# Optimization experiments

Hardware: AMD Instinct MI355X
Metric: run time of the kernel (lower is better)

Reference implementation:

```python
import jax, jax.numpy as jnp
import numpy as np

B, Ng, A, Eg = 32, 2500, 50, 2000      # graphs, atoms/graph, residues/graph, edges/graph
DIN, EDIM, H1, H2, AF, HG = 64, 16, 64, 64, 95, 128
F1, F2, F3 = 64, 32, 16
K, T = 3, 6                             # ARMA num_stacks, num_layers
N, E = B * Ng, B * Eg


def _glorot(k, shape, fan_in):
    return jax.random.normal(k, shape, jnp.float32) / np.sqrt(fan_in)


def setup_inputs():
    key = jax.random.key(0)
    ks = jax.random.split(key, 24)
    x = jax.random.normal(ks[0], (N, DIN), jnp.float32)
    off = (jnp.arange(B) * Ng)[:, None]
    src = (jax.random.randint(ks[1], (B, Eg), 0, Ng) + off).reshape(-1)
    dst = (jax.random.randint(ks[2], (B, Eg), 0, Ng) + off).reshape(-1)
    edge_index = jnp.stack([src, dst])
    edge_attr = jax.random.normal(ks[3], (E, EDIM), jnp.float32)
    monomer_labels = jnp.tile(jnp.arange(Ng) // (Ng // A), B)  # atom -> residue (0..A-1, per graph)
    aminoacids_features = jax.random.normal(ks[4], (B, A, AF), jnp.float32)
    FIN = H2 + AF  # 159, ARMA input dim
    return {
        'x': x, 'edge_index': edge_index, 'edge_attr': edge_attr,
        'monomer_labels': monomer_labels, 'aminoacids_features': aminoacids_features,
        'w_e1': _glorot(ks[5], (EDIM, DIN * H1), EDIM), 'b_e1': jnp.zeros((DIN * H1,)),
        'root1': _glorot(ks[6], (DIN, H1), DIN), 'bias1': jnp.zeros((H1,)),
        'w_e2': _glorot(ks[7], (EDIM, H1 * H2), EDIM), 'b_e2': jnp.zeros((H1 * H2,)),
        'root2': _glorot(ks[8], (H1, H2), H1), 'bias2': jnp.zeros((H2,)),
        'attn_atom_w': _glorot(ks[9], (H2, 1), H2), 'attn_atom_b': jnp.zeros((1,)),
        'arma_init_w': _glorot(ks[10], (K, FIN, HG), FIN),
        'arma_w': _glorot(ks[11], (T - 1, K, HG, HG), HG),
        'arma_root_w': _glorot(ks[12], (T, K, FIN, HG), FIN),
        'arma_bias': jnp.zeros((T, K, 1, HG)),
        'attn_aa_w': _glorot(ks[13], (HG, 1), HG), 'attn_aa_b': jnp.zeros((1,)),
        'w1': _glorot(ks[14], (HG, F1), HG), 'b1': jnp.zeros((F1,)),
        'w2': _glorot(ks[15], (F1, F2), F1), 'b2': jnp.zeros((F2,)),
        'w3': _glorot(ks[16], (F2, F3), F2), 'b3': jnp.zeros((F3,)),
        'w4': _glorot(ks[17], (F3, 1), F3), 'b4': jnp.zeros((1,)),
    }


def reference(x, edge_index, edge_attr, monomer_labels, aminoacids_features,
              w_e1, b_e1, root1, bias1, w_e2, b_e2, root2, bias2,
              attn_atom_w, attn_atom_b, arma_init_w, arma_w, arma_root_w, arma_bias,
              attn_aa_w, attn_aa_b, w1, b1, w2, b2, w3, b3, w4, b4):
    src, dst = edge_index[0], edge_index[1]

    def nnconv(h, w_e, b_e, root, bias):
        din, dout = root.shape
        W = (edge_attr @ w_e + b_e).reshape(-1, din, dout)      # per-edge weight [E, din, dout]
        msg = jnp.einsum('ei,eio->eo', h[src], W)               # per-edge matvec
        agg = jax.ops.segment_sum(msg, dst, num_segments=N)     # scatter-add at dst
        return agg + h @ root + bias

    h = jax.nn.relu(nnconv(x, w_e1, b_e1, root1, bias1))
    h = jax.nn.relu(nnconv(h, w_e2, b_e2, root2, bias2))

    # AttentionReadoutAtom per graph: softmax over atoms, scatter-sum to residues
    hb = h.reshape(B, Ng, H2)
    attn = jax.nn.softmax(hb @ attn_atom_w + attn_atom_b, axis=1)
    wx = (hb * attn).reshape(-1, H2)
    seg = (monomer_labels.reshape(B, Ng) + jnp.arange(B)[:, None] * A).reshape(-1)
    amino = jax.ops.segment_sum(wx, seg, num_segments=B * A).reshape(B, A, H2)
    xi = jnp.concatenate([amino, aminoacids_features], axis=-1)  # [B, A, H2+95]

    # ARMAConv over directed residue chain i->i+1; gcn_norm w/o self-loops:
    # node 0 has in-degree 0 so edge (0,1) gets norm 0, all others norm 1.
    norm = jnp.concatenate([jnp.zeros(1), jnp.ones(A - 2)])      # [A-1]

    def prop(z):  # z: [B, K, A, F]; out[i+1] = norm_i * z[i]
        shifted = z[..., :-1, :] * norm[:, None]
        return jnp.concatenate([jnp.zeros_like(z[..., :1, :]), shifted], axis=-2)

    out = prop(jnp.einsum('baf,kfg->bkag', xi, arma_init_w))
    out = jax.nn.relu(out + jnp.einsum('baf,kfg->bkag', xi, arma_root_w[0]) + arma_bias[0][None])
    for t in range(1, T):
        out = prop(jnp.einsum('bkaf,kfg->bkag', out, arma_w[t - 1]))
        out = jax.nn.relu(out + jnp.einsum('baf,kfg->bkag', xi, arma_root_w[t]) + arma_bias[t][None])
    g = jax.nn.relu(out.mean(axis=1))  # mean over K stacks -> [B, A, HG]

    # AttentionReadoutAminoAcid: softmax over residues, weighted sum
    a = jax.nn.softmax(g @ attn_aa_w + attn_aa_b, axis=1)
    p = (g * a).sum(axis=1)  # [B, HG]

    # MLP head (dropout is identity in eval mode)
    p = jax.nn.relu(p @ w1 + b1)
    p = jax.nn.relu(p @ w2 + b2)
    p = jax.nn.relu(p @ w3 + b3)
    return (p @ w4 + b4).reshape(-1)
```

## Files before the change

### kernel.cpp

```cpp
#include <hip/hip_runtime.h>

#define N_NODES 80000
#define N_EDGES 64000
#define NB      32
#define NG      2500
#define NA      50
#define EDIM    16
#define FIN     159
#define HG      128
#define RICOLS  2688

typedef __attribute__((ext_vector_type(8))) short bf16x8;
typedef __attribute__((ext_vector_type(4))) float f32x4;

__device__ inline ushort rne_bf16(float f) {
    union { float f; unsigned u; } v; v.f = f;
    const unsigned r = v.u + 0x7fffu + ((v.u >> 16) & 1u);
    return (ushort)(r >> 16);
}
__device__ inline float bf16_to_f32(ushort h) {
    union { unsigned u; float f; } v; v.u = ((unsigned)h) << 16;
    return v.f;
}
__device__ __forceinline__ void gl_lds16(const void* gsrc, void* ldst) {
    __builtin_amdgcn_global_load_lds(
        (const __attribute__((address_space(1))) unsigned int*)gsrc,
        (__attribute__((address_space(3))) unsigned int*)ldst, 16, 0, 0);
}

__global__ __launch_bounds__(256) void prep_all(const float* __restrict__ we1, const float* __restrict__ be1,
    const float* __restrict__ we2, const float* __restrict__ be2, const float* __restrict__ armaw,
    ushort* __restrict__ w1h, ushort* __restrict__ w1l, ushort* __restrict__ w2h, ushort* __restrict__ w2l,
    ushort* __restrict__ abh, ushort* __restrict__ abl)
{
    const int b = blockIdx.x;
    if (b < 68) {
        int idx = b * 256 + threadIdx.x;
        const int half = (idx >= 17 * 8 * 64) ? 1 : 0;
        if (half) idx -= 17 * 8 * 64;
        if (idx >= 17 * 8 * 64) return;
        const float* we = half ? we2 : we1;
        const float* be = half ? be2 : be1;
        ushort* Wh = half ? w2h : w1h;
        ushort* Wlo = half ? w2l : w1l;
        const int l = idx & 63;
        const int slot = (idx >> 6) & 7;
        const int j = idx >> 9;
        const int n = slot >> 1, kq = slot & 1;
        const int o = n * 16 + (l & 15);
        const int i0 = kq * 32 + (l >> 4) * 8;
        ushort th[8], tl[8];
#pragma unroll
        for (int t = 0; t < 8; ++t) {
            const int i = i0 + t;
            const float f = (j < 16) ? we[j * 4096 + i * 64 + o] : be[i * 64 + o];
            const ushort hi = rne_bf16(f);
            th[t] = hi;
            tl[t] = rne_bf16(f - bf16_to_f32(hi));
        }
        *(uint4*)(Wh + (size_t)idx * 8) = *(const uint4*)th;
        *(uint4*)(Wlo + (size_t)idx * 8) = *(const uint4*)tl;
    } else {
        const int idx = (b - 68) * 256 + threadIdx.x;
        if (idx >= 15 * 32 * 64) return;
        const int l = idx & 63;
        const int slot = (idx >> 6) & 31;
        const int ws = idx >> 11;
        const int n = slot >> 2, kt = slot & 3;
        const int c = n * 16 + (l & 15);
        const int f0 = kt * 32 + (l >> 4) * 8;
        ushort th[8], tl[8];
#pragma unroll
        for (int t = 0; t < 8; ++t) {
            const float v = armaw[(size_t)ws * 16384 + (size_t)(f0 + t) * 128 + c];
            const ushort hi = rne_bf16(v);
            th[t] = hi;
            tl[t] = rne_bf16(v - bf16_to_f32(hi));
        }
        *(uint4*)(abh + (size_t)idx * 8) = *(const uint4*)th;
        *(uint4*)(abl + (size_t)idx * 8) = *(const uint4*)tl;
    }
}

template<int RELU>
__global__ __launch_bounds__(256) void root_gemm(const float* __restrict__ in,
    const float* __restrict__ w, const float* __restrict__ bias, float* __restrict__ out)
{
    __shared__ float At[64 * 65];
    __shared__ float Wl[64 * 64];
    __shared__ float bl[64];
    const int tid = threadIdx.x;
    const int r0 = blockIdx.x * 64;
    for (int s = tid; s < 4096; s += 256) {
        int r = s >> 6, c = s & 63;
        float v = in[(r0 + r) * 64 + c];
        if (RELU) v = fmaxf(v, 0.f);
        At[c * 65 + r] = v;
    }
    for (int s = tid; s < 4096; s += 256) Wl[s] = w[s];
    if (tid < 64) bl[tid] = bias[tid];
    __syncthreads();
    const int tr = tid >> 4, tc = tid & 15;
    float acc[4][4] = {};
#pragma unroll 8
    for (int i = 0; i < 64; ++i) {
        const float4 a4 = *(const float4*)&At[i * 65 + tr * 4];
        const float4 b4 = *(const float4*)&Wl[i * 64 + tc * 4];
        const float av[4] = {a4.x, a4.y, a4.z, a4.w};
        const float bv[4] = {b4.x, b4.y, b4.z, b4.w};
#pragma unroll
        for (int m = 0; m < 4; ++m)
#pragma unroll
            for (int n = 0; n < 4; ++n) acc[m][n] = fmaf(av[m], bv[n], acc[m][n]);
    }
    const float4 bq = *(const float4*)&bl[tc * 4];
#pragma unroll
    for (int m = 0; m < 4; ++m) {
        float4 o4 = {acc[m][0] + bq.x, acc[m][1] + bq.y, acc[m][2] + bq.z, acc[m][3] + bq.w};
        *(float4*)&out[(r0 + tr * 4 + m) * 64 + tc * 4] = o4;
    }
}

#define TE 128
template<int RELU>
__global__ __launch_bounds__(256) void edge_conv_mfma(const float* __restrict__ h,
    const float* __restrict__ ea, const int* __restrict__ src, const int* __restrict__ dst,
    const ushort* __restrict__ Whi, const ushort* __restrict__ Wlo, float* __restrict__ agg)
{
    __shared__ ushort Bst[2][8192];
    __shared__ float  EAt[17 * 132];
    const int tid = threadIdx.x;
    const int e0 = blockIdx.x * TE;
    const int wv = tid >> 6, l = tid & 63;

#pragma unroll
    for (int i = 0; i < 4; ++i) {
        const int c = wv * 4 + i;
        const ushort* gs = (c < 8) ? (Whi + ((size_t)c * 64 + l) * 8)
                                   : (Wlo + ((size_t)(c - 8) * 64 + l) * 8);
        gl_lds16(gs, (char*)(&Bst[0][0]) + c * 1024);
    }
    for (int s = tid; s < TE * 16; s += 256) {
        const int le = s >> 4, j = s & 15;
        EAt[j * 132 + le] = ea[(size_t)(e0 + le) * 16 + j];
    }
    if (tid < TE) EAt[16 * 132 + tid] = 1.0f;

    bf16x8 ah[2][2], al[2][2];
#pragma unroll
    for (int m = 0; m < 2; ++m) {
        const int erow = wv * 32 + m * 16 + (l & 15);
        const int nd = src[e0 + erow];
        const float4* hp = (const float4*)(h + (size_t)nd * 64);
#pragma unroll
        for (int kq = 0; kq < 2; ++kq) {
            const int q0 = kq * 8 + (l >> 4) * 2;
            const float4 v0 = hp[q0], v1 = hp[q0 + 1];
            const float fv[8] = {v0.x, v0.y, v0.z, v0.w, v1.x, v1.y, v1.z, v1.w};
            ushort th[8], tl[8];
#pragma unroll
            for (int t = 0; t < 8; ++t) {
                const float f = RELU ? fmaxf(fv[t], 0.f) : fv[t];
                th[t] = rne_bf16(f);
                tl[t] = rne_bf16(f - bf16_to_f32(th[t]));
            }
            ah[m][kq] = *(const bf16x8*)th;
            al[m][kq] = *(const bf16x8*)tl;
        }
    }
    __syncthreads();

    f32x4 msg[2][4];
#pragma unroll
    for (int m = 0; m < 2; ++m)
#pragma unroll
        for (int n = 0; n < 4; ++n) msg[m][n] = (f32x4)0.f;

#pragma unroll 1
    for (int j = 0; j < 17; ++j) {
        const int cur = j & 1;
        if (j < 16) {
#pragma unroll
            for (int i = 0; i < 4; ++i) {
                const int c = wv * 4 + i;
                const ushort* gs = (c < 8) ? (Whi + ((size_t)((j + 1) * 8 + c) * 64 + l) * 8)
                                           : (Wlo + ((size_t)((j + 1) * 8 + (c - 8)) * 64 + l) * 8);
                gl_lds16(gs, (char*)(&Bst[cur ^ 1][0]) + c * 1024);
            }
        }
        f32x4 eam[2];
        eam[0] = *(const f32x4*)&EAt[j * 132 + wv * 32 + (l >> 4) * 4];
        eam[1] = *(const f32x4*)&EAt[j * 132 + wv * 32 + 16 + (l >> 4) * 4];
#pragma unroll
        for (int n = 0; n < 4; ++n) {
            const char* bb = (const char*)(&Bst[cur][0]);
            const bf16x8 bh0 = *(const bf16x8*)(bb + ((n * 2 + 0) * 64 + l) * 16);
            const bf16x8 bh1 = *(const bf16x8*)(bb + ((n * 2 + 1) * 64 + l) * 16);
            const bf16x8 bl0 = *(const bf16x8*)(bb + 8192 + ((n * 2 + 0) * 64 + l) * 16);
            const bf16x8 bl1 = *(const bf16x8*)(bb + 8192 + ((n * 2 + 1) * 64 + l) * 16);
#pragma unroll
            for (int m = 0; m < 2; ++m) {
                f32x4 t = __builtin_amdgcn_mfma_f32_16x16x32_bf16(ah[m][0], bh0, (f32x4)0.f, 0, 0, 0);
                t = __builtin_amdgcn_mfma_f32_16x16x32_bf16(ah[m][1], bh1, t, 0, 0, 0);
                t = __builtin_amdgcn_mfma_f32_16x16x32_bf16(ah[m][0], bl0, t, 0, 0, 0);
                t = __builtin_amdgcn_mfma_f32_16x16x32_bf16(ah[m][1], bl1, t, 0, 0, 0);
                t = __builtin_amdgcn_mfma_f32_16x16x32_bf16(al[m][0], bh0, t, 0, 0, 0);
                t = __builtin_amdgcn_mfma_f32_16x16x32_bf16(al[m][1], bh1, t, 0, 0, 0);
                msg[m][n] += eam[m] * t;
            }
        }
        __syncthreads();
    }

#pragma unroll
    for (int m = 0; m < 2; ++m)
#pragma unroll
        for (int r = 0; r < 4; ++r) {
            const int erow = wv * 32 + m * 16 + (l >> 4) * 4 + r;
            const size_t d = (size_t)dst[e0 + erow] * 64;
#pragma unroll
            for (int n = 0; n < 4; ++n)
                atomicAdd(&agg[d + n * 16 + (l & 15)], msg[m][n][r]);
        }
}

__global__ __launch_bounds__(256) void scores_k(const float* __restrict__ h2,
    const float* __restrict__ w, const float* __restrict__ b, float* __restrict__ sc)
{
    __shared__ float wl[64];
    if (threadIdx.x < 64) wl[threadIdx.x] = w[threadIdx.x];
    __syncthreads();
    const int n = blockIdx.x * 256 + threadIdx.x;
    if (n < N_NODES) {
        float acc = b[0];
        const float4* hp = (const float4*)(h2 + (long)n * 64);
#pragma unroll
        for (int q = 0; q < 16; ++q) {
            const float4 v = hp[q];
            acc = fmaf(fmaxf(v.x, 0.f), wl[q * 4 + 0], acc); acc = fmaf(fmaxf(v.y, 0.f), wl[q * 4 + 1], acc);
            acc = fmaf(fmaxf(v.z, 0.f), wl[q * 4 + 2], acc); acc = fmaf(fmaxf(v.w, 0.f), wl[q * 4 + 3], acc);
        }
        sc[n] = acc;
    }
}

__global__ __launch_bounds__(256) void softmax_k(const float* __restrict__ sc, float* __restrict__ attn)
{
    __shared__ float red[256];
    const int g = blockIdx.x, tid = threadIdx.x;
    const float* s = sc + (long)g * NG;
    float m = -1e30f;
    for (int a = tid; a < NG; a += 256) m = fmaxf(m, s[a]);
    red[tid] = m; __syncthreads();
    for (int st = 128; st; st >>= 1) { if (tid < st) red[tid] = fmaxf(red[tid], red[tid + st]); __syncthreads(); }
    const float mx = red[0]; __syncthreads();
    float sum = 0.f;
    for (int a = tid; a < NG; a += 256) sum += expf(s[a] - mx);
    red[tid] = sum; __syncthreads();
    for (int st = 128; st; st >>= 1) { if (tid < st) red[tid] += red[tid + st]; __syncthreads(); }
    const float inv = 1.0f / red[0];
    for (int a = tid; a < NG; a += 256) attn[(long)g * NG + a] = expf(s[a] - mx) * inv;
}

__global__ __launch_bounds__(256) void amino_k(const float* __restrict__ h2,
    const float* __restrict__ attn, const float* __restrict__ aa, float* __restrict__ xi)
{
    const int tid = threadIdx.x;
    const int r = blockIdx.x * 4 + (tid >> 6);
    const int o = tid & 63;
    const int g = r / NA, ar = r % NA;
    const long base = (long)g * NG + ar * 50;
    float acc = 0.f;
#pragma unroll 10
    for (int a = 0; a < 50; ++a) acc = fmaf(attn[base + a], fmaxf(h2[(base + a) * 64 + o], 0.f), acc);
    xi[(long)r * FIN + o] = acc;
    for (int s = tid; s < 4 * 95; s += 256) {
        const int lr = s / 95, f = s % 95;
        const int rr = blockIdx.x * 4 + lr;
        xi[(long)rr * FIN + 64 + f] = aa[(long)rr * 95 + f];
    }
}

__global__ __launch_bounds__(256) void ri_gemm(const float* __restrict__ xi,
    const float* __restrict__ rootw, const float* __restrict__ initw,
    const float* __restrict__ abias, float* __restrict__ RI)
{
    __shared__ float At[32 * 65];
    __shared__ float Bl[32 * 64];
    const int tid = threadIdx.x;
    const int r0 = blockIdx.x * 64, c0 = blockIdx.y * 64;
    const int blk = c0 >> 7;
    const int gb = c0 & 127;
    const float* bsrc = (blk < 18) ? (rootw + (long)blk * FIN * 128) : (initw + (long)(blk - 18) * FIN * 128);
    const int tr = tid >> 4, tc = tid & 15;
    float acc[4][4] = {};
    for (int f0 = 0; f0 < FIN; f0 += 32) {
        __syncthreads();
        for (int s = tid; s < 64 * 32; s += 256) {
            const int r = s >> 5, kk = s & 31; const int f = f0 + kk;
            At[kk * 65 + r] = (f < FIN) ? xi[(long)(r0 + r) * FIN + f] : 0.f;
        }
        for (int s = tid; s < 32 * 64; s += 256) {
            const int kk = s >> 6, cc = s & 63; const int f = f0 + kk;
            Bl[s] = (f < FIN) ? bsrc[(long)f * 128 + gb + cc] : 0.f;
        }
        __syncthreads();
#pragma unroll 8
        for (int kk = 0; kk < 32; ++kk) {
            const float4 a4 = *(const float4*)&At[kk * 65 + tr * 4];
            const float4 b4 = *(const float4*)&Bl[kk * 64 + tc * 4];
            const float av[4] = {a4.x, a4.y, a4.z, a4.w};
            const float bv[4] = {b4.x, b4.y, b4.z, b4.w};
#pragma unroll
            for (int m = 0; m < 4; ++m)
#pragma unroll
                for (int n = 0; n < 4; ++n) acc[m][n] = fmaf(av[m], bv[n], acc[m][n]);
        }
    }
    float4 bq = {0.f, 0.f, 0.f, 0.f};
    if (blk < 18) bq = *(const float4*)&abias[c0 + tc * 4];
#pragma unroll
    for (int m = 0; m < 4; ++m) {
        float4 o4 = {acc[m][0] + bq.x, acc[m][1] + bq.y, acc[m][2] + bq.z, acc[m][3] + bq.w};
        *(float4*)&RI[(long)(r0 + tr * 4 + m) * RICOLS + c0 + tc * 4] = o4;
    }
}

__global__ __launch_bounds__(64) void arma_mfma(const float* __restrict__ RI,
    const ushort* __restrict__ Bh, const ushort* __restrict__ Bl, float* __restrict__ G)
{
    __shared__ float X[16 * 132];
    const int bid = blockIdx.x;
    const int chunk = bid % 5;
    const int gk = bid / 5;
    const int k = gk % 3, g = gk / 3;
    const int s0 = chunk * 11 - 5;
    const size_t rbase = (size_t)g * NA;
    const int l = threadIdx.x;

    for (int s = l; s < 16 * 128; s += 64) {
        const int lr = s >> 7, o = s & 127;
        const int a = s0 + lr;
        float v = 0.f;
        if (a >= 0 && a < NA) {
            v = RI[(rbase + a) * RICOLS + k * 128 + o];
            if (a >= 2) v += RI[(rbase + a - 1) * RICOLS + (18 + k) * 128 + o];
            v = fmaxf(v, 0.f);
        }
        X[lr * 132 + o] = v;
    }

    const int arow = l & 15;
    const int aabs = s0 + arow;
    const bool avalid = (arow >= 1) && (aabs >= 2) && (aabs < NA);
    const int srow = avalid ? (arow - 1) : arow;

#pragma unroll 1
    for (int t = 1; t <= 5; ++t) {
        bf16x8 ah[4], al[4];
#pragma unroll
        for (int kt = 0; kt < 4; ++kt) {
            const float* xp = &X[srow * 132 + kt * 32 + (l >> 4) * 8];
            const float4 v0 = *(const float4*)xp;
            const float4 v1 = *(const float4*)(xp + 4);
            const float fv[8] = {v0.x, v0.y, v0.z, v0.w, v1.x, v1.y, v1.z, v1.w};
            ushort th[8], tl[8];
#pragma unroll
            for (int t8 = 0; t8 < 8; ++t8) {
                const float f = avalid ? fv[t8] : 0.f;
                th[t8] = rne_bf16(f);
                tl[t8] = rne_bf16(f - bf16_to_f32(th[t8]));
            }
            ah[kt] = *(const bf16x8*)th;
            al[kt] = *(const bf16x8*)tl;
        }
        f32x4 acc[8];
#pragma unroll
        for (int n = 0; n < 8; ++n) acc[n] = (f32x4)0.f;
        const size_t wb = (size_t)(((t - 1) * 3 + k) * 32) * 512;
#pragma unroll
        for (int kt = 0; kt < 4; ++kt) {
            bf16x8 bh8[8], bl8[8];
#pragma unroll
            for (int n = 0; n < 8; ++n) {
                const size_t fo = wb + (size_t)(n * 4 + kt) * 512 + (size_t)l * 8;
                bh8[n] = *(const bf16x8*)(Bh + fo);
                bl8[n] = *(const bf16x8*)(Bl + fo);
            }
#pragma unroll
            for (int n = 0; n < 8; ++n) {
                acc[n] = __builtin_amdgcn_mfma_f32_16x16x32_bf16(ah[kt], bh8[n], acc[n], 0, 0, 0);
                acc[n] = __builtin_amdgcn_mfma_f32_16x16x32_bf16(ah[kt], bl8[n], acc[n], 0, 0, 0);
                acc[n] = __builtin_amdgcn_mfma_f32_16x16x32_bf16(al[kt], bh8[n], acc[n], 0, 0, 0);
            }
        }
#pragma unroll
        for (int n = 0; n < 8; ++n) {
            const int col = n * 16 + (l & 15);
#pragma unroll
            for (int r = 0; r < 4; ++r) {
                const int crow = (l >> 4) * 4 + r;
                const int ca = s0 + crow;
                float v = 0.f;
                if (ca >= 0 && ca < NA) {
                    const float rv = RI[(rbase + ca) * RICOLS + (t * 3 + k) * 128 + col];
                    v = fmaxf(acc[n][r] + rv, 0.f);
                }
                X[crow * 132 + col] = v;
            }
        }
    }

    const int nout = (chunk == 4) ? 6 : 11;
    for (int s = l; s < nout * 128; s += 64) {
        const int lr = 5 + (s >> 7), o = s & 127;
        G[((size_t)k * 1600 + rbase + (size_t)(s0 + lr)) * 128 + o] = X[lr * 132 + o];
    }
}

__global__ __launch_bounds__(256) void final_k(const float* __restrict__ G,
    const float* __restrict__ waa, const float* __restrict__ baa,
    const float* __restrict__ w1, const float* __restrict__ b1,
    const float* __restrict__ w2, const float* __restrict__ b2,
    const float* __restrict__ w3, const float* __restrict__ b3,
    const float* __restrict__ w4, const float* __restrict__ b4, float* __restrict__ out)
{
    __shared__ float gl[50 * 129];
    __shared__ float sc[64];
    __shared__ float pl[128];
    __shared__ float h1l[64], h2l[32], h3l[16];
    __shared__ float wl[128];
    const int b = blockIdx.x, tid = threadIdx.x;
    for (int s = tid; s < 50 * 128; s += 256) {
        const int a = s >> 7, o = s & 127;
        const size_t r = ((size_t)b * 50 + a) * 128 + o;
        const float v = (G[r] + G[(size_t)1600 * 128 + r] + G[(size_t)2 * 1600 * 128 + r]) * (1.f / 3.f);
        gl[a * 129 + o] = fmaxf(v, 0.f);
    }
    if (tid < 128) wl[tid] = waa[tid];
    __syncthreads();
    if (tid < 50) {
        float acc = baa[0];
        for (int f = 0; f < 128; ++f) acc = fmaf(gl[tid * 129 + f], wl[f], acc);
        sc[tid] = acc;
    }
    __syncthreads();
    if (tid < 64) {
        const float v = (tid < 50) ? sc[tid] : -1e30f;
        float m = v;
        for (int d = 32; d; d >>= 1) m = fmaxf(m, __shfl_xor(m, d));
        const float e = (tid < 50) ? expf(v - m) : 0.f;
        float ssum = e;
        for (int d = 32; d; d >>= 1) ssum += __shfl_xor(ssum, d);
        if (tid < 50) sc[tid] = e / ssum;
    }
    __syncthreads();
    if (tid < 128) {
        float acc = 0.f;
        for (int a = 0; a < 50; ++a) acc = fmaf(sc[a], gl[a * 129 + tid], acc);
        pl[tid] = acc;
    }
    __syncthreads();
    if (tid < 64) {
        float acc = b1[tid];
        for (int f = 0; f < 128; ++f) acc = fmaf(pl[f], w1[f * 64 + tid], acc);
        h1l[tid] = fmaxf(acc, 0.f);
    }
    __syncthreads();
    if (tid < 32) {
        float acc = b2[tid];
        for (int f = 0; f < 64; ++f) acc = fmaf(h1l[f], w2[f * 32 + tid], acc);
        h2l[tid] = fmaxf(acc, 0.f);
    }
    __syncthreads();
    if (tid < 16) {
        float acc = b3[tid];
        for (int f = 0; f < 32; ++f) acc = fmaf(h2l[f], w3[f * 16 + tid], acc);
        h3l[tid] = fmaxf(acc, 0.f);
    }
    __syncthreads();
    if (tid == 0) {
        float acc = b4[0];
        for (int f = 0; f < 16; ++f) acc = fmaf(h3l[f], w4[f], acc);
        out[b] = acc;
    }
}

extern "C" void kernel_launch(void* const* d_in, const int* in_sizes, int n_in,
                              void* d_out, int out_size, void* d_ws, size_t ws_size,
                              hipStream_t stream) {
    const float* x     = (const float*)d_in[0];
    const int*   eidx  = (const int*)d_in[1];
    const float* ea    = (const float*)d_in[2];
    const float* aaf   = (const float*)d_in[4];
    const float* we1   = (const float*)d_in[5];
    const float* be1   = (const float*)d_in[6];
    const float* root1 = (const float*)d_in[7];
    const float* bias1 = (const float*)d_in[8];
    const float* we2   = (const float*)d_in[9];
    const float* be2   = (const float*)d_in[10];
    const float* root2 = (const float*)d_in[11];
    const float* bias2 = (const float*)d_in[12];
    const float* waw   = (const float*)d_in[13];
    const float* wab   = (const float*)d_in[14];
    const float* initw = (const float*)d_in[15];
    const float* armaw = (const float*)d_in[16];
    const float* rootw = (const float*)d_in[17];
    const float* abias = (const float*)d_in[18];
    const float* waa   = (const float*)d_in[19];
    const float* baa   = (const float*)d_in[20];
    const float* w1    = (const float*)d_in[21];
    const float* b1    = (const float*)d_in[22];
    const float* w2    = (const float*)d_in[23];
    const float* b2    = (const float*)d_in[24];
    const float* w3    = (const float*)d_in[25];
    const float* b3    = (const float*)d_in[26];
    const float* w4    = (const float*)d_in[27];
    const float* b4    = (const float*)d_in[28];
    float* out = (float*)d_out;

    const int* src = eidx;
    const int* dst = eidx + N_EDGES;

    char* ws = (char*)d_ws;
    size_t off = 0;
    float* h1     = (float*)(ws + off); off += (size_t)N_NODES * 64 * 4;
    float* h2     = (float*)(ws + off); off += (size_t)N_NODES * 64 * 4;
    float* scores = (float*)(ws + off); off += (size_t)N_NODES * 4;
    float* attn   = (float*)(ws + off); off += (size_t)N_NODES * 4;
    float* xi     = (float*)(ws + off); off += (size_t)1600 * FIN * 4;
    float* RI     = (float*)(ws + off); off += (size_t)1600 * RICOLS * 4;
    float* G      = (float*)(ws + off); off += (size_t)3 * 1600 * 128 * 4;
    ushort* wt1h  = (ushort*)(ws + off); off += (size_t)17 * 8 * 64 * 8 * 2;
    ushort* wt1l  = (ushort*)(ws + off); off += (size_t)17 * 8 * 64 * 8 * 2;
    ushort* wt2h  = (ushort*)(ws + off); off += (size_t)17 * 8 * 64 * 8 * 2;
    ushort* wt2l  = (ushort*)(ws + off); off += (size_t)17 * 8 * 64 * 8 * 2;
    ushort* abh   = (ushort*)(ws + off); off += (size_t)15 * 32 * 64 * 8 * 2;
    ushort* abl   = (ushort*)(ws + off); off += (size_t)15 * 32 * 64 * 8 * 2;

    prep_all<<<188, 256, 0, stream>>>(we1, be1, we2, be2, armaw, wt1h, wt1l, wt2h, wt2l, abh, abl);

    root_gemm<0><<<N_NODES / 64, 256, 0, stream>>>(x, root1, bias1, h1);
    edge_conv_mfma<0><<<N_EDGES / TE, 256, 0, stream>>>(x, ea, src, dst, wt1h, wt1l, h1);
    root_gemm<1><<<N_NODES / 64, 256, 0, stream>>>(h1, root2, bias2, h2);
    edge_conv_mfma<1><<<N_EDGES / TE, 256, 0, stream>>>(h1, ea, src, dst, wt2h, wt2l, h2);
    scores_k<<<(N_NODES + 255) / 256, 256, 0, stream>>>(h2, waw, wab, scores);
    softmax_k<<<NB, 256, 0, stream>>>(scores, attn);
    amino_k<<<1600 / 4, 256, 0, stream>>>(h2, attn, aaf, xi);
    ri_gemm<<<dim3(25, 42), 256, 0, stream>>>(xi, rootw, initw, abias, RI);
    arma_mfma<<<NB * 3 * 5, 64, 0, stream>>>(RI, abh, abl, G);
    final_k<<<NB, 256, 0, stream>>>(G, waa, baa, w1, b1, w2, b2, w3, b3, w4, b4, out);
}
```

Baseline: 363.1 us.

## Split fused ARMA recurrence into per-step MFMA kernels with banked RI layout

Replaces the single ARMA kernel, which ran all five recurrence steps in one block per 11-row chunk with halo recomputation, by five launches of a per-step kernel over a (row tile, column group, stack) grid that ping-pongs XA/XB buffers through global memory. The RI output of ri_gemm is relaid out into contiguous 128-column banks so each step reads its slice with unit stride. This removes halo redundancy and exposes far more blocks (1200 per step instead of 480), at the cost of four extra kernel launches and global round-trips of the intermediate state.

```diff
diff --git a/kernel.cpp b/kernel.cpp
--- a/kernel.cpp
+++ b/kernel.cpp
@@ -8,7 +8,7 @@
 #define EDIM    16
 #define FIN     159
 #define HG      128
-#define RICOLS  2688
+#define NBANKS  21
 
 typedef __attribute__((ext_vector_type(8))) short bf16x8;
 typedef __attribute__((ext_vector_type(4))) float f32x4;
@@ -283,7 +283,7 @@
 
 __global__ __launch_bounds__(256) void ri_gemm(const float* __restrict__ xi,
     const float* __restrict__ rootw, const float* __restrict__ initw,
-    const float* __restrict__ abias, float* __restrict__ RI)
+    const float* __restrict__ abias, float* __restrict__ RI2)
 {
     __shared__ float At[32 * 65];
     __shared__ float Bl[32 * 64];
@@ -322,99 +322,87 @@
 #pragma unroll
     for (int m = 0; m < 4; ++m) {
         float4 o4 = {acc[m][0] + bq.x, acc[m][1] + bq.y, acc[m][2] + bq.z, acc[m][3] + bq.w};
-        *(float4*)&RI[(long)(r0 + tr * 4 + m) * RICOLS + c0 + tc * 4] = o4;
-    }
-}
-
-__global__ __launch_bounds__(64) void arma_mfma(const float* __restrict__ RI,
-    const ushort* __restrict__ Bh, const ushort* __restrict__ Bl, float* __restrict__ G)
-{
-    __shared__ float X[16 * 132];
-    const int bid = blockIdx.x;
-    const int chunk = bid % 5;
-    const int gk = bid / 5;
-    const int k = gk % 3, g = gk / 3;
-    const int s0 = chunk * 11 - 5;
-    const size_t rbase = (size_t)g * NA;
+        *(float4*)&RI2[((size_t)blk * 1600 + (r0 + tr * 4 + m)) * 128 + gb + tc * 4] = o4;
+    }
+}
+
+template<int INIT>
+__global__ __launch_bounds__(64) void arma_step_mfma(const float* __restrict__ Xin,
+    const float* __restrict__ RI2, const ushort* __restrict__ Bh, const ushort* __restrict__ Bl,
+    float* __restrict__ Xout, int t)
+{
+    const int rt = blockIdx.x, cg = blockIdx.y, k = blockIdx.z;
     const int l = threadIdx.x;
-
-    for (int s = l; s < 16 * 128; s += 64) {
-        const int lr = s >> 7, o = s & 127;
-        const int a = s0 + lr;
-        float v = 0.f;
-        if (a >= 0 && a < NA) {
-            v = RI[(rbase + a) * RICOLS + k * 128 + o];
-            if (a >= 2) v += RI[(rbase + a - 1) * RICOLS + (18 + k) * 128 + o];
-            v = fmaxf(v, 0.f);
-        }
-        X[lr * 132 + o] = v;
-    }
-
-    const int arow = l & 15;
-    const int aabs = s0 + arow;
-    const bool avalid = (arow >= 1) && (aabs >= 2) && (aabs < NA);
-    const int srow = avalid ? (arow - 1) : arow;
-
-#pragma unroll 1
-    for (int t = 1; t <= 5; ++t) {
-        bf16x8 ah[4], al[4];
-#pragma unroll
-        for (int kt = 0; kt < 4; ++kt) {
-            const float* xp = &X[srow * 132 + kt * 32 + (l >> 4) * 8];
-            const float4 v0 = *(const float4*)xp;
-            const float4 v1 = *(const float4*)(xp + 4);
-            const float fv[8] = {v0.x, v0.y, v0.z, v0.w, v1.x, v1.y, v1.z, v1.w};
-            ushort th[8], tl[8];
-#pragma unroll
-            for (int t8 = 0; t8 < 8; ++t8) {
-                const float f = avalid ? fv[t8] : 0.f;
-                th[t8] = rne_bf16(f);
-                tl[t8] = rne_bf16(f - bf16_to_f32(th[t8]));
-            }
-            ah[kt] = *(const bf16x8*)th;
-            al[kt] = *(const bf16x8*)tl;
-        }
-        f32x4 acc[8];
-#pragma unroll
-        for (int n = 0; n < 8; ++n) acc[n] = (f32x4)0.f;
-        const size_t wb = (size_t)(((t - 1) * 3 + k) * 32) * 512;
-#pragma unroll
-        for (int kt = 0; kt < 4; ++kt) {
-            bf16x8 bh8[8], bl8[8];
-#pragma unroll
-            for (int n = 0; n < 8; ++n) {
-                const size_t fo = wb + (size_t)(n * 4 + kt) * 512 + (size_t)l * 8;
-                bh8[n] = *(const bf16x8*)(Bh + fo);
-                bl8[n] = *(const bf16x8*)(Bl + fo);
-            }
-#pragma unroll
-            for (int n = 0; n < 8; ++n) {
-                acc[n] = __builtin_amdgcn_mfma_f32_16x16x32_bf16(ah[kt], bh8[n], acc[n], 0, 0, 0);
-                acc[n] = __builtin_amdgcn_mfma_f32_16x16x32_bf16(ah[kt], bl8[n], acc[n], 0, 0, 0);
-                acc[n] = __builtin_amdgcn_mfma_f32_16x16x32_bf16(al[kt], bh8[n], acc[n], 0, 0, 0);
-            }
-        }
-#pragma unroll
-        for (int n = 0; n < 8; ++n) {
-            const int col = n * 16 + (l & 15);
-#pragma unroll
-            for (int r = 0; r < 4; ++r) {
-                const int crow = (l >> 4) * 4 + r;
-                const int ca = s0 + crow;
-                float v = 0.f;
-                if (ca >= 0 && ca < NA) {
-                    const float rv = RI[(rbase + ca) * RICOLS + (t * 3 + k) * 128 + col];
-                    v = fmaxf(acc[n][r] + rv, 0.f);
-                }
-                X[crow * 132 + col] = v;
-            }
-        }
-    }
-
-    const int nout = (chunk == 4) ? 6 : 11;
-    for (int s = l; s < nout * 128; s += 64) {
-        const int lr = 5 + (s >> 7), o = s & 127;
-        G[((size_t)k * 1600 + rbase + (size_t)(s0 + lr)) * 128 + o] = X[lr * 132 + o];
+    const int r0 = rt * 16;
+
+    const int ar = r0 + (l & 15);
+    const int aa = ar % NA;
+    const bool avalid = (aa >= 2);
+    const int asrc = avalid ? (ar - 1) : ar;
+    bf16x8 ah[4], al[4];
+#pragma unroll
+    for (int kt = 0; kt < 4; ++kt) {
+        const int coff = kt * 32 + (l >> 4) * 8;
+        float fv[8];
+        if (INIT) {
+            const float4 u0 = *(const float4*)(RI2 + ((size_t)k * 1600 + asrc) * 128 + coff);
+            const float4 u1 = *(const float4*)(RI2 + ((size_t)k * 1600 + asrc) * 128 + coff + 4);
+            const int psrc = (asrc >= 1) ? (asrc - 1) : 0;
+            const float4 p0 = *(const float4*)(RI2 + ((size_t)(18 + k) * 1600 + psrc) * 128 + coff);
+            const float4 p1 = *(const float4*)(RI2 + ((size_t)(18 + k) * 1600 + psrc) * 128 + coff + 4);
+            const float pm = (aa >= 3) ? 1.f : 0.f;
+            fv[0] = fmaxf(u0.x + pm * p0.x, 0.f); fv[1] = fmaxf(u0.y + pm * p0.y, 0.f);
+            fv[2] = fmaxf(u0.z + pm * p0.z, 0.f); fv[3] = fmaxf(u0.w + pm * p0.w, 0.f);
+            fv[4] = fmaxf(u1.x + pm * p1.x, 0.f); fv[5] = fmaxf(u1.y + pm * p1.y, 0.f);
+            fv[6] = fmaxf(u1.z + pm * p1.z, 0.f); fv[7] = fmaxf(u1.w + pm * p1.w, 0.f);
+        } else {
+            const float4 u0 = *(const float4*)(Xin + ((size_t)k * 1600 + asrc) * 128 + coff);
+            const float4 u1 = *(const float4*)(Xin + ((size_t)k * 1600 + asrc) * 128 + coff + 4);
+            fv[0] = u0.x; fv[1] = u0.y; fv[2] = u0.z; fv[3] = u0.w;
+            fv[4] = u1.x; fv[5] = u1.y; fv[6] = u1.z; fv[7] = u1.w;
+        }
+        ushort th[8], tl[8];
+#pragma unroll
+        for (int t8 = 0; t8 < 8; ++t8) {
+            const float f = avalid ? fv[t8] : 0.f;
+            th[t8] = rne_bf16(f);
+            tl[t8] = rne_bf16(f - bf16_to_f32(th[t8]));
+        }
+        ah[kt] = *(const bf16x8*)th;
+        al[kt] = *(const bf16x8*)tl;
+    }
+
+    f32x4 acc[2];
+    acc[0] = (f32x4)0.f; acc[1] = (f32x4)0.f;
+    const size_t wb = (size_t)(((t - 1) * 3 + k) * 32) * 512;
+#pragma unroll
+    for (int kt = 0; kt < 4; ++kt) {
+        bf16x8 bh2[2], bl2[2];
+#pragma unroll
+        for (int n2 = 0; n2 < 2; ++n2) {
+            const int n = cg * 2 + n2;
+            const size_t fo = wb + (size_t)(n * 4 + kt) * 512 + (size_t)l * 8;
+            bh2[n2] = *(const bf16x8*)(Bh + fo);
+            bl2[n2] = *(const bf16x8*)(Bl + fo);
+        }
+#pragma unroll
+        for (int n2 = 0; n2 < 2; ++n2) {
+            acc[n2] = __builtin_amdgcn_mfma_f32_16x16x32_bf16(ah[kt], bh2[n2], acc[n2], 0, 0, 0);
+            acc[n2] = __builtin_amdgcn_mfma_f32_16x16x32_bf16(ah[kt], bl2[n2], acc[n2], 0, 0, 0);
+            acc[n2] = __builtin_amdgcn_mfma_f32_16x16x32_bf16(al[kt], bh2[n2], acc[n2], 0, 0, 0);
+        }
+    }
+
+    const float* rroot = RI2 + (size_t)(t * 3 + k) * 1600 * 128;
+#pragma unroll
+    for (int n2 = 0; n2 < 2; ++n2) {
+        const int col = (cg * 2 + n2) * 16 + (l & 15);
+#pragma unroll
+        for (int r = 0; r < 4; ++r) {
+            const int crow = r0 + (l >> 4) * 4 + r;
+            const float rv = rroot[(size_t)crow * 128 + col];
+            Xout[((size_t)k * 1600 + crow) * 128 + col] = fmaxf(acc[n2][r] + rv, 0.f);
+        }
     }
 }
 
@@ -529,7 +517,9 @@
     float* scores = (float*)(ws + off); off += (size_t)N_NODES * 4;
     float* attn   = (float*)(ws + off); off += (size_t)N_NODES * 4;
     float* xi     = (float*)(ws + off); off += (size_t)1600 * FIN * 4;
-    float* RI     = (float*)(ws + off); off += (size_t)1600 * RICOLS * 4;
+    float* RI2    = (float*)(ws + off); off += (size_t)NBANKS * 1600 * 128 * 4;
+    float* XA     = (float*)(ws + off); off += (size_t)3 * 1600 * 128 * 4;
+    float* XB     = (float*)(ws + off); off += (size_t)3 * 1600 * 128 * 4;
     float* G      = (float*)(ws + off); off += (size_t)3 * 1600 * 128 * 4;
     ushort* wt1h  = (ushort*)(ws + off); off += (size_t)17 * 8 * 64 * 8 * 2;
     ushort* wt1l  = (ushort*)(ws + off); off += (size_t)17 * 8 * 64 * 8 * 2;
@@ -547,7 +537,12 @@
     scores_k<<<(N_NODES + 255) / 256, 256, 0, stream>>>(h2, waw, wab, scores);
     softmax_k<<<NB, 256, 0, stream>>>(scores, attn);
     amino_k<<<1600 / 4, 256, 0, stream>>>(h2, attn, aaf, xi);
-    ri_gemm<<<dim3(25, 42), 256, 0, stream>>>(xi, rootw, initw, abias, RI);
-    arma_mfma<<<NB * 3 * 5, 64, 0, stream>>>(RI, abh, abl, G);
+    ri_gemm<<<dim3(25, 42), 256, 0, stream>>>(xi, rootw, initw, abias, RI2);
+    const dim3 agrid(100, 4, 3);
+    arma_step_mfma<1><<<agrid, 64, 0, stream>>>(XB, RI2, abh, abl, XA, 1);
+    arma_step_mfma<0><<<agrid, 64, 0, stream>>>(XA, RI2, abh, abl, XB, 2);
+    arma_step_mfma<0><<<agrid, 64, 0, stream>>>(XB, RI2, abh, abl, XA, 3);
+    arma_step_mfma<0><<<agrid, 64, 0, stream>>>(XA, RI2, abh, abl, XB, 4);
+    arma_step_mfma<0><<<agrid, 64, 0, stream>>>(XB, RI2, abh, abl, G, 5);
     final_k<<<NB, 256, 0, stream>>>(G, waa, baa, w1, b1, w2, b2, w3, b3, w4, b4, out);
 }
```

Result: faster. 319.2 us (-12.1%).
